# Performance work log

Measured on AMD Instinct MI355X. Metric: run time of the kernel, lower is better.

Reference implementation:

```python
import jax, jax.numpy as jnp
import numpy as np

K = 10          # neighbors, hard-coded in MLP1.forward
NEG_SLOPE = 0.2 # LeakyReLU slope
EPS = 1e-5      # BatchNorm2d default eps


def setup_inputs() -> dict:
    key = jax.random.key(0)
    k1, k2, k3, k4 = jax.random.split(key, 4)
    B, C, N = 8, 6, 4096
    x = jax.random.normal(k1, (B, C, N), dtype=jnp.float32)
    W = jax.random.normal(k2, (64, 6), dtype=jnp.float32) * 0.2      # conv1x1 weight (O, I)
    gamma = jax.random.uniform(k3, (64,), jnp.float32, 0.5, 1.5)     # BN weight
    beta = jax.random.normal(k4, (64,), dtype=jnp.float32) * 0.1     # BN bias
    return {"x": x, "W": W, "gamma": gamma, "beta": beta}


def _knn_idx(x3, k):
    # pairwise_distance[b,i,j] = -||x_i - x_j||^2 (as in the torch knn)
    inner = jnp.einsum('bdn,bdm->bnm', x3, x3)          # x_i . x_j
    xx = jnp.sum(x3 * x3, axis=1)                       # (B, N)
    pd = 2.0 * inner - xx[:, :, None] - xx[:, None, :]  # (B, N, N)
    _, idx = jax.lax.top_k(pd, k)                       # k nearest (incl. self)
    return idx                                          # (B, N, k) int32


def reference(x, W, gamma, beta):
    # x: (B, 6, N)
    idx = _knn_idx(x[:, :3], K)                          # (B, N, k)
    # gather neighbor features: feat[b,c,n,j] = x[b,c,idx[b,n,j]]
    feat = jax.vmap(lambda xb, ib: xb[:, ib])(x, idx)    # (B, 6, N, k)
    # center xyz over the k neighbors and scale by 10
    xyz = feat[:, :3]
    xyz = (xyz - jnp.mean(xyz, axis=-1, keepdims=True)) * 10.0
    feat = jnp.concatenate([xyz, feat[:, 3:]], axis=1)   # (B, 6, N, k)
    # 1x1 conv (6 -> 64), no bias
    y = jnp.einsum('oc,bcnk->bonk', W, feat)             # (B, 64, N, k)
    # BatchNorm2d in train mode: batch stats over (B, N, k), biased variance
    mu = jnp.mean(y, axis=(0, 2, 3), keepdims=True)
    var = jnp.mean((y - mu) ** 2, axis=(0, 2, 3), keepdims=True)
    y = (y - mu) * jax.lax.rsqrt(var + EPS)
    y = y * gamma[None, :, None, None] + beta[None, :, None, None]
    # LeakyReLU(0.2)
    y = jnp.where(y >= 0, y, NEG_SLOPE * y)
    # max over neighbors k
    y = jnp.max(y, axis=-1)                              # (B, 64, N)
    # global max + mean pooling over N, concat along last axis
    x1 = jnp.max(y, axis=-1)                             # (B, 64)
    x2 = jnp.mean(y, axis=-1)                            # (B, 64)
    return jnp.concatenate([x1, x2], axis=-1)            # (B, 128)
```

## Files before the change

kernel.cpp:

```cpp
#include <hip/hip_runtime.h>
#include <float.h>

#define K_NN 10
#define BATCH 8
#define CIN 6
#define NPTS 4096
#define COUT 64
#define NSEG 8
#define SEGLEN (NPTS / NSEG)
#define CHUNK 16
#define NCHUNK (SEGLEN / CHUNK)
#define NWORD (SEGLEN / 32)
#define NEG_SLOPE 0.2f
#define BN_EPS 1e-5f

static constexpr size_t OFF_PTS  = 0;
static constexpr size_t OFF_PTS2 = OFF_PTS + (size_t)BATCH * NPTS * sizeof(float4);
static constexpr size_t OFF_Q    = OFF_PTS2 + (size_t)BATCH * NPTS * sizeof(float4);
static constexpr size_t OFF_ST   = OFF_Q + (size_t)BATCH * COUT * NPTS * sizeof(float);

__device__ __forceinline__ float wave_sum(float v) {
#pragma unroll
    for (int m = 32; m >= 1; m >>= 1) v += __shfl_xor(v, m, 64);
    return v;
}
__device__ __forceinline__ float wave_max(float v) {
#pragma unroll
    for (int m = 32; m >= 1; m >>= 1) v = fmaxf(v, __shfl_xor(v, m, 64));
    return v;
}

__device__ __forceinline__ float distp(float qx, float qy, float qz, float4 c) {
    return fmaf(c.x, qx, fmaf(c.y, qy, fmaf(c.z, qz, -c.w)));
}

__device__ __forceinline__ float fmax3(float a, float b, float c) {
    return fmaxf(fmaxf(a, b), c);
}

#define CHL(cj) { float _hi = fmaxf(cj, t); t = fminf(cj, t); cj = _hi; }

#define CSWP(va, vb, ia, ib) \
    if (va > vb) { float _tv = va; va = vb; vb = _tv; int _ti = ia; ia = ib; ib = _ti; }

#define INSERT10(dd, mm) \
    if ((dd) > v9) { \
        v9 = (dd); i9 = (mm); \
        CSWP(v9, v8, i9, i8) \
        CSWP(v8, v7, i8, i7) \
        CSWP(v7, v6, i7, i6) \
        CSWP(v6, v5, i6, i5) \
        CSWP(v5, v4, i5, i4) \
        CSWP(v4, v3, i4, i3) \
        CSWP(v3, v2, i3, i2) \
        CSWP(v2, v1, i2, i1) \
        CSWP(v1, v0, i1, i0) \
    }

__global__ __launch_bounds__(256) void prep_pts(const float* __restrict__ x,
                                                float4* __restrict__ pts,
                                                float4* __restrict__ pts2,
                                                double* __restrict__ stats) {
    if (blockIdx.x == 0 && threadIdx.x < 27) stats[threadIdx.x] = 0.0;
    int t = blockIdx.x * 256 + threadIdx.x;
    int b = t >> 12;
    int n = t & (NPTS - 1);
    const float* xb = x + (size_t)b * CIN * NPTS;
    float x0 = xb[n];
    float x1 = xb[NPTS + n];
    float x2 = xb[2 * NPTS + n];
    pts[t] = make_float4(2.0f * x0, 2.0f * x1, 2.0f * x2, x0 * x0 + x1 * x1 + x2 * x2);
    float x3 = xb[3 * NPTS + n];
    float x4 = xb[4 * NPTS + n];
    float x5 = xb[5 * NPTS + n];
    pts2[t] = make_float4(x3, x4, x5, 0.0f);
}

__global__ __launch_bounds__(512, 4) void knnmf_kernel(const float4* __restrict__ pts,
                                                       const float4* __restrict__ pts2,
                                                       const float* __restrict__ W,
                                                       float* __restrict__ q,
                                                       double* __restrict__ stats) {
    __shared__ float dml[NSEG][K_NN][64];
    __shared__ unsigned short iml[NSEG][K_NN][64];
    __shared__ unsigned short idxL[K_NN][64];
    __shared__ float sW[COUT * CIN];
    __shared__ float sstat[27];

    for (int i = threadIdx.x; i < COUT * CIN; i += 512) sW[i] = W[i];

    int b  = blockIdx.y;
    int ln = threadIdx.x & 63;
    int wv = threadIdx.x >> 6;
    int wvu = __builtin_amdgcn_readfirstlane(wv);
    int n  = blockIdx.x * 64 + ln;
    const float4* p = pts + (size_t)b * NPTS;
    float4 q4 = p[n];
    float qx = 0.5f * q4.x, qy = 0.5f * q4.y, qz = 0.5f * q4.z;
    int m0 = wvu * SEGLEN;

    {
        float c0 = -FLT_MAX, c1 = -FLT_MAX, c2 = -FLT_MAX, c3 = -FLT_MAX, c4 = -FLT_MAX;
        float c5 = -FLT_MAX, c6 = -FLT_MAX, c7 = -FLT_MAX, c8 = -FLT_MAX, c9 = -FLT_MAX;

        for (int ch = 0; ch < NCHUNK; ch++) {
            const float4* cp = p + (m0 + ch * CHUNK);
            float d0  = distp(qx, qy, qz, cp[0]);
            float d1  = distp(qx, qy, qz, cp[1]);
            float d2  = distp(qx, qy, qz, cp[2]);
            float d3  = distp(qx, qy, qz, cp[3]);
            float d4  = distp(qx, qy, qz, cp[4]);
            float d5  = distp(qx, qy, qz, cp[5]);
            float d6  = distp(qx, qy, qz, cp[6]);
            float d7  = distp(qx, qy, qz, cp[7]);
            float d8  = distp(qx, qy, qz, cp[8]);
            float d9  = distp(qx, qy, qz, cp[9]);
            float d10 = distp(qx, qy, qz, cp[10]);
            float d11 = distp(qx, qy, qz, cp[11]);
            float d12 = distp(qx, qy, qz, cp[12]);
            float d13 = distp(qx, qy, qz, cp[13]);
            float d14 = distp(qx, qy, qz, cp[14]);
            float d15 = distp(qx, qy, qz, cp[15]);
            float a0 = fmax3(d0, d1, d2);
            float a1 = fmax3(d3, d4, d5);
            float a2 = fmax3(d6, d7, d8);
            float a3 = fmax3(d9, d10, d11);
            float a4 = fmax3(d12, d13, d14);
            float t = fmaxf(fmax3(fmax3(a0, a1, a2), a3, a4), d15);
            CHL(c0) CHL(c1) CHL(c2) CHL(c3) CHL(c4)
            CHL(c5) CHL(c6) CHL(c7) CHL(c8) CHL(c9)
        }
        float thr = c9;

        float v0 = -FLT_MAX, v1 = -FLT_MAX, v2 = -FLT_MAX, v3 = -FLT_MAX, v4 = -FLT_MAX;
        float v5 = -FLT_MAX, v6 = -FLT_MAX, v7 = -FLT_MAX, v8 = -FLT_MAX, v9 = -FLT_MAX;
        int i0 = 0, i1 = 0, i2 = 0, i3 = 0, i4 = 0;
        int i5 = 0, i6 = 0, i7 = 0, i8 = 0, i9 = 0;

        for (int w = 0; w < NWORD; w++) {
            const float4* cp = p + (m0 + w * 32);
            unsigned int mask = 0u;
#pragma unroll
            for (int u = 0; u < 32; u++) {
                float d = distp(qx, qy, qz, cp[u]);
                mask = (mask << 1) | (d >= thr ? 1u : 0u);
            }
            int base = m0 + w * 32;
            while (mask) {
                int j = __builtin_clz(mask);
                mask ^= (0x80000000u >> j);
                int m = base + j;
                float4 cc = p[m];
                float d = distp(qx, qy, qz, cc);
                INSERT10(d, m)
            }
        }

        dml[wv][0][ln] = v0; iml[wv][0][ln] = (unsigned short)i0;
        dml[wv][1][ln] = v1; iml[wv][1][ln] = (unsigned short)i1;
        dml[wv][2][ln] = v2; iml[wv][2][ln] = (unsigned short)i2;
        dml[wv][3][ln] = v3; iml[wv][3][ln] = (unsigned short)i3;
        dml[wv][4][ln] = v4; iml[wv][4][ln] = (unsigned short)i4;
        dml[wv][5][ln] = v5; iml[wv][5][ln] = (unsigned short)i5;
        dml[wv][6][ln] = v6; iml[wv][6][ln] = (unsigned short)i6;
        dml[wv][7][ln] = v7; iml[wv][7][ln] = (unsigned short)i7;
        dml[wv][8][ln] = v8; iml[wv][8][ln] = (unsigned short)i8;
        dml[wv][9][ln] = v9; iml[wv][9][ln] = (unsigned short)i9;
    }
    __syncthreads();

    if (wvu == 0) {
        float v0 = -FLT_MAX, v1 = -FLT_MAX, v2 = -FLT_MAX, v3 = -FLT_MAX, v4 = -FLT_MAX;
        float v5 = -FLT_MAX, v6 = -FLT_MAX, v7 = -FLT_MAX, v8 = -FLT_MAX, v9 = -FLT_MAX;
        int i0 = 0, i1 = 0, i2 = 0, i3 = 0, i4 = 0;
        int i5 = 0, i6 = 0, i7 = 0, i8 = 0, i9 = 0;
#pragma unroll
        for (int w = 0; w < NSEG; w++) {
#pragma unroll
            for (int j = 0; j < K_NN; j++) {
                float d = dml[w][j][ln];
                int m = iml[w][j][ln];
                INSERT10(d, m)
            }
        }
        idxL[0][ln] = (unsigned short)i0;
        idxL[1][ln] = (unsigned short)i1;
        idxL[2][ln] = (unsigned short)i2;
        idxL[3][ln] = (unsigned short)i3;
        idxL[4][ln] = (unsigned short)i4;
        idxL[5][ln] = (unsigned short)i5;
        idxL[6][ln] = (unsigned short)i6;
        idxL[7][ln] = (unsigned short)i7;
        idxL[8][ln] = (unsigned short)i8;
        idxL[9][ln] = (unsigned short)i9;
    }
    __syncthreads();

    const float4* p2 = pts2 + (size_t)b * NPTS;

    int nb[K_NN];
#pragma unroll
    for (int k = 0; k < K_NN; k++) nb[k] = idxL[k][ln];

    float f[CIN][K_NN];
#pragma unroll
    for (int k = 0; k < K_NN; k++) {
        float4 c = p[nb[k]];
        f[0][k] = 0.5f * c.x; f[1][k] = 0.5f * c.y; f[2][k] = 0.5f * c.z;
    }
#pragma unroll
    for (int k = 0; k < K_NN; k++) {
        float4 c2 = p2[nb[k]];
        f[3][k] = c2.x; f[4][k] = c2.y; f[5][k] = c2.z;
    }

#pragma unroll
    for (int c = 0; c < 3; c++) {
        float s = 0.f;
#pragma unroll
        for (int k = 0; k < K_NN; k++) s += f[c][k];
        float m = s / 10.0f;
#pragma unroll
        for (int k = 0; k < K_NN; k++) f[c][k] = (f[c][k] - m) * 10.0f;
    }

    float* qb = q + (size_t)b * COUT * NPTS + n;
    int o0 = wvu * 8;
#pragma unroll
    for (int oo = 0; oo < 8; oo++) {
        int o = o0 + oo;
        float w0 = sW[o * 6 + 0], w1 = sW[o * 6 + 1], w2 = sW[o * 6 + 2];
        float w3 = sW[o * 6 + 3], w4 = sW[o * 6 + 4], w5 = sW[o * 6 + 5];
        float mx = -FLT_MAX;
#pragma unroll
        for (int k = 0; k < K_NN; k++) {
            float y = w0 * f[0][k] + w1 * f[1][k] + w2 * f[2][k] +
                      w3 * f[3][k] + w4 * f[4][k] + w5 * f[5][k];
            mx = fmaxf(mx, y);
        }
        qb[(size_t)o * NPTS] = mx;
    }

    if (wvu == 0) {
        float s1[CIN];
#pragma unroll
        for (int c = 0; c < CIN; c++) {
            float s = 0.f;
#pragma unroll
            for (int k = 0; k < K_NN; k++) s += f[c][k];
            s1[c] = s;
        }
        float s2[21];
#pragma unroll
        for (int i = 0; i < 21; i++) s2[i] = 0.f;
#pragma unroll
        for (int k = 0; k < K_NN; k++) {
            int pp = 0;
#pragma unroll
            for (int c = 0; c < CIN; c++)
#pragma unroll
                for (int c2 = c; c2 < CIN; c2++) {
                    s2[pp] += f[c][k] * f[c2][k];
                    pp++;
                }
        }
#pragma unroll
        for (int c = 0; c < CIN; c++) s1[c] = wave_sum(s1[c]);
#pragma unroll
        for (int i = 0; i < 21; i++) s2[i] = wave_sum(s2[i]);

        if (ln == 0) {
#pragma unroll
            for (int c = 0; c < CIN; c++) sstat[c] = s1[c];
#pragma unroll
            for (int i = 0; i < 21; i++) sstat[6 + i] = s2[i];
        }
        if (ln < 27) atomicAdd(&stats[ln], (double)sstat[ln]);
    }
}

__global__ __launch_bounds__(256) void reduce_kernel(const float* __restrict__ q,
                                                     const double* __restrict__ stats,
                                                     const float* __restrict__ W,
                                                     const float* __restrict__ gamma,
                                                     const float* __restrict__ beta,
                                                     float* __restrict__ out) {
    int o = blockIdx.x;
    int b = blockIdx.y;

    __shared__ float s_sc, s_sh;
    if (threadIdx.x == 0) {
        const double minv = 1.0 / (double)((size_t)BATCH * NPTS * K_NN);
        double w[CIN];
#pragma unroll
        for (int c = 0; c < CIN; c++) w[c] = (double)W[o * CIN + c];
        double mu = 0.0;
#pragma unroll
        for (int c = 0; c < CIN; c++) mu += w[c] * stats[c];
        mu *= minv;
        double ey2 = 0.0;
        int pp = 6;
#pragma unroll
        for (int c = 0; c < CIN; c++)
#pragma unroll
            for (int c2 = c; c2 < CIN; c2++) {
                double v = w[c] * w[c2] * stats[pp];
                ey2 += (c2 == c) ? v : 2.0 * v;
                pp++;
            }
        ey2 *= minv;
        double var = ey2 - mu * mu;
        float scale = gamma[o] * rsqrtf((float)var + BN_EPS);
        float shift = beta[o] - (float)mu * scale;
        s_sc = scale;
        s_sh = shift;
    }
    __syncthreads();
    float scale = s_sc, shift = s_sh;

    const float* qp = q + ((size_t)b * COUT + o) * NPTS;
    float mx = -FLT_MAX, sm = 0.f;
    for (int i = threadIdx.x; i < NPTS; i += 256) {
        float z = scale * qp[i] + shift;
        z = (z >= 0.f) ? z : NEG_SLOPE * z;
        mx = fmaxf(mx, z);
        sm += z;
    }
    mx = wave_max(mx);
    sm = wave_sum(sm);
    __shared__ float smx[4], ssm2[4];
    int wv = threadIdx.x >> 6;
    int ln = threadIdx.x & 63;
    if (ln == 0) { smx[wv] = mx; ssm2[wv] = sm; }
    __syncthreads();
    if (threadIdx.x == 0) {
        float m = fmaxf(fmaxf(smx[0], smx[1]), fmaxf(smx[2], smx[3]));
        float s = ssm2[0] + ssm2[1] + ssm2[2] + ssm2[3];
        out[b * 2 * COUT + o] = m;
        out[b * 2 * COUT + COUT + o] = s * (1.0f / (float)NPTS);
    }
}

extern "C" void kernel_launch(void* const* d_in, const int* in_sizes, int n_in,
                              void* d_out, int out_size, void* d_ws, size_t ws_size,
                              hipStream_t stream) {
    const float* x     = (const float*)d_in[0];
    const float* W     = (const float*)d_in[1];
    const float* gamma = (const float*)d_in[2];
    const float* beta  = (const float*)d_in[3];
    float* out = (float*)d_out;

    char* ws = (char*)d_ws;
    float4* pts   = (float4*)(ws + OFF_PTS);
    float4* pts2  = (float4*)(ws + OFF_PTS2);
    float*  q     = (float*)(ws + OFF_Q);
    double* stats = (double*)(ws + OFF_ST);

    prep_pts<<<BATCH * NPTS / 256, 256, 0, stream>>>(x, pts, pts2, stats);
    knnmf_kernel<<<dim3(NPTS / 64, BATCH), 512, 0, stream>>>(pts, pts2, W, q, stats);
    reduce_kernel<<<dim3(COUT, BATCH), 256, 0, stream>>>(q, stats, W, gamma, beta, out);
}
```

Before: 165.7 us.

## Use packed-FP32 pair layout for KNN distance scans

Measured after the change: 163.8 us. No clear change (-1.2%).

```diff
diff --git a/kernel.cpp b/kernel.cpp
--- a/kernel.cpp
+++ b/kernel.cpp
@@ -16,8 +16,11 @@
 
 static constexpr size_t OFF_PTS  = 0;
 static constexpr size_t OFF_PTS2 = OFF_PTS + (size_t)BATCH * NPTS * sizeof(float4);
-static constexpr size_t OFF_Q    = OFF_PTS2 + (size_t)BATCH * NPTS * sizeof(float4);
+static constexpr size_t OFF_PTSP = OFF_PTS2 + (size_t)BATCH * NPTS * sizeof(float4);
+static constexpr size_t OFF_Q    = OFF_PTSP + (size_t)BATCH * NPTS * sizeof(float4);
 static constexpr size_t OFF_ST   = OFF_Q + (size_t)BATCH * COUT * NPTS * sizeof(float);
+
+typedef float v2f __attribute__((ext_vector_type(2)));
 
 __device__ __forceinline__ float wave_sum(float v) {
 #pragma unroll
@@ -34,8 +37,27 @@
     return fmaf(c.x, qx, fmaf(c.y, qy, fmaf(c.z, qz, -c.w)));
 }
 
-__device__ __forceinline__ float fmax3(float a, float b, float c) {
-    return fmaxf(fmaxf(a, b), c);
+__device__ __forceinline__ v2f dist2(v2f qx2, v2f qy2, v2f qz2, float4 fa, float4 fb) {
+    v2f cx = {fa.x, fa.y}, cy = {fa.z, fa.w}, cz = {fb.x, fb.y}, cw = {fb.z, fb.w};
+#if __has_builtin(__builtin_elementwise_fma)
+    v2f t = __builtin_elementwise_fma(cz, qz2, -cw);
+    t = __builtin_elementwise_fma(cy, qy2, t);
+    t = __builtin_elementwise_fma(cx, qx2, t);
+    return t;
+#else
+    v2f t;
+    t[0] = fmaf(cx[0], qx2[0], fmaf(cy[0], qy2[0], fmaf(cz[0], qz2[0], -cw[0])));
+    t[1] = fmaf(cx[1], qx2[1], fmaf(cy[1], qy2[1], fmaf(cz[1], qz2[1], -cw[1])));
+    return t;
+#endif
+}
+
+__device__ __forceinline__ v2f vmax2(v2f a, v2f b) {
+#if __has_builtin(__builtin_elementwise_max)
+    return __builtin_elementwise_max(a, b);
+#else
+    v2f r; r[0] = fmaxf(a[0], b[0]); r[1] = fmaxf(a[1], b[1]); return r;
+#endif
 }
 
 #define CHL(cj) { float _hi = fmaxf(cj, t); t = fminf(cj, t); cj = _hi; }
@@ -60,24 +82,36 @@
 __global__ __launch_bounds__(256) void prep_pts(const float* __restrict__ x,
                                                 float4* __restrict__ pts,
                                                 float4* __restrict__ pts2,
+                                                float4* __restrict__ ptsp,
                                                 double* __restrict__ stats) {
     if (blockIdx.x == 0 && threadIdx.x < 27) stats[threadIdx.x] = 0.0;
     int t = blockIdx.x * 256 + threadIdx.x;
     int b = t >> 12;
     int n = t & (NPTS - 1);
     const float* xb = x + (size_t)b * CIN * NPTS;
-    float x0 = xb[n];
-    float x1 = xb[NPTS + n];
-    float x2 = xb[2 * NPTS + n];
-    pts[t] = make_float4(2.0f * x0, 2.0f * x1, 2.0f * x2, x0 * x0 + x1 * x1 + x2 * x2);
+    float X = xb[n];
+    float Y = xb[NPTS + n];
+    float Z = xb[2 * NPTS + n];
+    float w = X * X + Y * Y + Z * Z;
+    pts[t] = make_float4(2.0f * X, 2.0f * Y, 2.0f * Z, w);
     float x3 = xb[3 * NPTS + n];
     float x4 = xb[4 * NPTS + n];
     float x5 = xb[5 * NPTS + n];
     pts2[t] = make_float4(x3, x4, x5, 0.0f);
+    float Xn = __shfl_down(X, 1, 64);
+    float Yn = __shfl_down(Y, 1, 64);
+    float Zn = __shfl_down(Z, 1, 64);
+    float wn = __shfl_down(w, 1, 64);
+    if ((n & 1) == 0) {
+        float4* pb = ptsp + (size_t)b * NPTS;
+        pb[n]     = make_float4(2.0f * X, 2.0f * Xn, 2.0f * Y, 2.0f * Yn);
+        pb[n + 1] = make_float4(2.0f * Z, 2.0f * Zn, w, wn);
+    }
 }
 
 __global__ __launch_bounds__(512, 4) void knnmf_kernel(const float4* __restrict__ pts,
                                                        const float4* __restrict__ pts2,
+                                                       const float4* __restrict__ ptsp,
                                                        const float* __restrict__ W,
                                                        float* __restrict__ q,
                                                        double* __restrict__ stats) {
@@ -94,9 +128,11 @@
     int wv = threadIdx.x >> 6;
     int wvu = __builtin_amdgcn_readfirstlane(wv);
     int n  = blockIdx.x * 64 + ln;
-    const float4* p = pts + (size_t)b * NPTS;
+    const float4* p   = pts  + (size_t)b * NPTS;
+    const float4* p2s = ptsp + (size_t)b * NPTS;
     float4 q4 = p[n];
     float qx = 0.5f * q4.x, qy = 0.5f * q4.y, qz = 0.5f * q4.z;
+    v2f qx2 = {qx, qx}, qy2 = {qy, qy}, qz2 = {qz, qz};
     int m0 = wvu * SEGLEN;
 
     {
@@ -104,29 +140,23 @@
         float c5 = -FLT_MAX, c6 = -FLT_MAX, c7 = -FLT_MAX, c8 = -FLT_MAX, c9 = -FLT_MAX;
 
         for (int ch = 0; ch < NCHUNK; ch++) {
-            const float4* cp = p + (m0 + ch * CHUNK);
-            float d0  = distp(qx, qy, qz, cp[0]);
-            float d1  = distp(qx, qy, qz, cp[1]);
-            float d2  = distp(qx, qy, qz, cp[2]);
-            float d3  = distp(qx, qy, qz, cp[3]);
-            float d4  = distp(qx, qy, qz, cp[4]);
-            float d5  = distp(qx, qy, qz, cp[5]);
-            float d6  = distp(qx, qy, qz, cp[6]);
-            float d7  = distp(qx, qy, qz, cp[7]);
-            float d8  = distp(qx, qy, qz, cp[8]);
-            float d9  = distp(qx, qy, qz, cp[9]);
-            float d10 = distp(qx, qy, qz, cp[10]);
-            float d11 = distp(qx, qy, qz, cp[11]);
-            float d12 = distp(qx, qy, qz, cp[12]);
-            float d13 = distp(qx, qy, qz, cp[13]);
-            float d14 = distp(qx, qy, qz, cp[14]);
-            float d15 = distp(qx, qy, qz, cp[15]);
-            float a0 = fmax3(d0, d1, d2);
-            float a1 = fmax3(d3, d4, d5);
-            float a2 = fmax3(d6, d7, d8);
-            float a3 = fmax3(d9, d10, d11);
-            float a4 = fmax3(d12, d13, d14);
-            float t = fmaxf(fmax3(fmax3(a0, a1, a2), a3, a4), d15);
+            const float4* cp = p2s + (m0 + ch * CHUNK);
+            v2f e0 = dist2(qx2, qy2, qz2, cp[0],  cp[1]);
+            v2f e1 = dist2(qx2, qy2, qz2, cp[2],  cp[3]);
+            v2f e2 = dist2(qx2, qy2, qz2, cp[4],  cp[5]);
+            v2f e3 = dist2(qx2, qy2, qz2, cp[6],  cp[7]);
+            v2f e4 = dist2(qx2, qy2, qz2, cp[8],  cp[9]);
+            v2f e5 = dist2(qx2, qy2, qz2, cp[10], cp[11]);
+            v2f e6 = dist2(qx2, qy2, qz2, cp[12], cp[13]);
+            v2f e7 = dist2(qx2, qy2, qz2, cp[14], cp[15]);
+            v2f a0 = vmax2(e0, e1);
+            v2f a1 = vmax2(e2, e3);
+            v2f a2 = vmax2(e4, e5);
+            v2f a3 = vmax2(e6, e7);
+            v2f b0 = vmax2(a0, a1);
+            v2f b1 = vmax2(a2, a3);
+            v2f cm = vmax2(b0, b1);
+            float t = fmaxf(cm[0], cm[1]);
             CHL(c0) CHL(c1) CHL(c2) CHL(c3) CHL(c4)
             CHL(c5) CHL(c6) CHL(c7) CHL(c8) CHL(c9)
         }
@@ -138,12 +168,12 @@
         int i5 = 0, i6 = 0, i7 = 0, i8 = 0, i9 = 0;
 
         for (int w = 0; w < NWORD; w++) {
-            const float4* cp = p + (m0 + w * 32);
+            const float4* cp = p2s + (m0 + w * 32);
             unsigned int mask = 0u;
 #pragma unroll
-            for (int u = 0; u < 32; u++) {
-                float d = distp(qx, qy, qz, cp[u]);
-                mask = (mask << 1) | (d >= thr ? 1u : 0u);
+            for (int pr = 0; pr < 16; pr++) {
+                v2f d2v = dist2(qx2, qy2, qz2, cp[2 * pr], cp[2 * pr + 1]);
+                mask = (mask << 2) | (d2v[0] >= thr ? 2u : 0u) | (d2v[1] >= thr ? 1u : 0u);
             }
             int base = m0 + w * 32;
             while (mask) {
@@ -353,10 +383,11 @@
     char* ws = (char*)d_ws;
     float4* pts   = (float4*)(ws + OFF_PTS);
     float4* pts2  = (float4*)(ws + OFF_PTS2);
+    float4* ptsp  = (float4*)(ws + OFF_PTSP);
     float*  q     = (float*)(ws + OFF_Q);
     double* stats = (double*)(ws + OFF_ST);
 
-    prep_pts<<<BATCH * NPTS / 256, 256, 0, stream>>>(x, pts, pts2, stats);
-    knnmf_kernel<<<dim3(NPTS / 64, BATCH), 512, 0, stream>>>(pts, pts2, W, q, stats);
+    prep_pts<<<BATCH * NPTS / 256, 256, 0, stream>>>(x, pts, pts2, ptsp, stats);
+    knnmf_kernel<<<dim3(NPTS / 64, BATCH), 512, 0, stream>>>(pts, pts2, ptsp, W, q, stats);
     reduce_kernel<<<dim3(COUT, BATCH), 256, 0, stream>>>(q, stats, W, gamma, beta, out);
 }
```
